# Kernel optimization log

Hardware: AMD Instinct MI355X
Metric: run time of the kernel (lower is better)

## Reference

```python
import jax, jax.numpy as jnp
import numpy as np

NUM_EMBED = 1024
NUM_HEADS = 16
NUM_LAYER = 8
BLOCK_SIZE = 1024
VOCAB = 32000
B, T = 4, 1024
HEAD_SIZE = NUM_EMBED // NUM_HEADS


def _ln(x, g, b, eps=1e-5):
    mu = jnp.mean(x, axis=-1, keepdims=True)
    var = jnp.var(x, axis=-1, keepdims=True)
    return (x - mu) * jax.lax.rsqrt(var + eps) * g + b


def setup_inputs() -> dict:
    key = jax.random.key(0)
    ks = jax.random.split(key, 16)
    C, L, V = NUM_EMBED, NUM_LAYER, VOCAB
    std = 0.02
    n = lambda k, shp: jax.random.normal(k, shp, jnp.float32) * std
    return {
        "x": jax.random.randint(ks[0], (B, T), 0, V),
        "tok_emb": n(ks[1], (V, C)),
        "pos_emb": n(ks[2], (BLOCK_SIZE, C)),
        "Wq": n(ks[3], (L, C, C)),
        "Wk": n(ks[4], (L, C, C)),
        "Wv": n(ks[5], (L, C, C)),
        "Wproj": n(ks[6], (L, C, C)),
        "bproj": jnp.zeros((L, C), jnp.float32),
        "ln1_g": jnp.ones((L, C), jnp.float32),
        "ln1_b": jnp.zeros((L, C), jnp.float32),
        "ln2_g": jnp.ones((L, C), jnp.float32),
        "ln2_b": jnp.zeros((L, C), jnp.float32),
        "W1": n(ks[7], (L, C, 4 * C)),
        "b1": jnp.zeros((L, 4 * C), jnp.float32),
        "W2": n(ks[8], (L, 4 * C, C)),
        "b2": jnp.zeros((L, C), jnp.float32),
        "lnf_g": jnp.ones((C,), jnp.float32),
        "lnf_b": jnp.zeros((C,), jnp.float32),
        "Whead": n(ks[9], (C, V)),
    }


def _forward(x, tok_emb, pos_emb, Wq, Wk, Wv, Wproj, bproj,
             ln1_g, ln1_b, ln2_g, ln2_b, W1, b1, W2, b2,
             lnf_g, lnf_b, Whead):
    Bc, Tc = x.shape
    H, hs = NUM_HEADS, HEAD_SIZE
    h = tok_emb[x] + pos_emb[:Tc]  # [B,T,C]
    causal = jnp.tril(jnp.ones((Tc, Tc), bool))
    neg_inf = jnp.finfo(h.dtype).min
    for l in range(NUM_LAYER):
        xn = _ln(h, ln1_g[l], ln1_b[l])
        q = (xn @ Wq[l]).reshape(Bc, Tc, H, hs)
        k = (xn @ Wk[l]).reshape(Bc, Tc, H, hs)
        v = (xn @ Wv[l]).reshape(Bc, Tc, H, hs)
        att = jnp.einsum('bqhd,bkhd->bhqk', q, k) * (hs ** -0.5)
        att = jnp.where(causal, att, neg_inf)
        att = jax.nn.softmax(att, axis=-1)  # dropout p=0 in eval
        o = jnp.einsum('bhqk,bkhd->bqhd', att, v).reshape(Bc, Tc, H * hs)
        h = h + o @ Wproj[l] + bproj[l]
        xn = _ln(h, ln2_g[l], ln2_b[l])
        h = h + jax.nn.relu(xn @ W1[l] + b1[l]) @ W2[l] + b2[l]
    h = _ln(h, lnf_g, lnf_b)
    return h @ Whead  # logits [B,T,V]


def reference(x, tok_emb, pos_emb, Wq, Wk, Wv, Wproj, bproj,
              ln1_g, ln1_b, ln2_g, ln2_b, W1, b1, W2, b2,
              lnf_g, lnf_b, Whead):
    return _forward(x, tok_emb, pos_emb, Wq, Wk, Wv, Wproj, bproj,
                    ln1_g, ln1_b, ln2_g, ln2_b, W1, b1, W2, b2,
                    lnf_g, lnf_b, Whead)
```

## Files before the change

kernel.cpp:

```cpp
#include <hip/hip_runtime.h>
#include <stdint.h>
#include <stddef.h>

#define C_DIM 1024
#define T_DIM 1024
#define B_DIM 4
#define L_DIM 8
#define V_DIM 32000
#define HS 64
#define NHEAD 16
#define NROWS (B_DIM * T_DIM)
#define LDQ   3072
#define PROWS 65536

typedef __bf16 bf16_t;
typedef __attribute__((ext_vector_type(8))) __bf16 bf16x8;
typedef __attribute__((ext_vector_type(4))) __bf16 bf16x4;
typedef __attribute__((ext_vector_type(4))) float f32x4;
typedef unsigned int u32;
typedef unsigned short u16;

static __device__ __forceinline__ f32x4 mfma16(bf16x8 a, bf16x8 b, f32x4 c) {
    return __builtin_amdgcn_mfma_f32_16x16x32_bf16(a, b, c, 0, 0, 0);
}

static __device__ __forceinline__ void gl_lds16(const bf16_t* g, bf16_t* l) {
    __builtin_amdgcn_global_load_lds(
        (const __attribute__((address_space(1))) u32*)(const void*)g,
        (__attribute__((address_space(3))) u32*)(void*)l, 16, 0, 0);
}

__global__ __launch_bounds__(256) void embed_kernel(
    const int* __restrict__ x, const float* __restrict__ tok,
    const float* __restrict__ pos, float* __restrict__ h) {
    int idx = blockIdx.x * 256 + threadIdx.x;
    int row = idx >> 8;
    int c4  = (idx & 255) * 4;
    int t   = row & (T_DIM - 1);
    int tk  = x[row];
    float4 a = *(const float4*)(tok + (size_t)tk * C_DIM + c4);
    float4 p = *(const float4*)(pos + (size_t)t * C_DIM + c4);
    float4 r;
    r.x = a.x + p.x; r.y = a.y + p.y; r.z = a.z + p.z; r.w = a.w + p.w;
    *(float4*)(h + (size_t)row * C_DIM + c4) = r;
}

static __device__ __forceinline__ void wtr_tile(
    const float* __restrict__ in, bf16_t* __restrict__ out,
    int K, int N, int n0, int k0, int tid) {
    __shared__ float t[64][65];
    int tx = tid & 63, tw = tid >> 6;
#pragma unroll 4
    for (int i = 0; i < 16; ++i) {
        int k = tw * 16 + i;
        t[k][tx] = in[(size_t)(k0 + k) * N + n0 + tx];
    }
    __syncthreads();
#pragma unroll 4
    for (int i = 0; i < 16; ++i) {
        int n = tw * 16 + i;
        out[(size_t)(n0 + n) * K + k0 + tx] = (bf16_t)t[tx][n];
    }
}

__global__ __launch_bounds__(256) void wtr_kernel(
    const float* __restrict__ in, bf16_t* __restrict__ out, int K, int N) {
    wtr_tile(in, out, K, N, blockIdx.x * 64, blockIdx.y * 64, threadIdx.x);
}

__global__ __launch_bounds__(256) void wtr_layer_kernel(
    const float* __restrict__ Wq, const float* __restrict__ Wk,
    const float* __restrict__ Wv, const float* __restrict__ Wp,
    const float* __restrict__ W1, const float* __restrict__ W2,
    bf16_t* __restrict__ qkvT, bf16_t* __restrict__ projT,
    bf16_t* __restrict__ w1T, bf16_t* __restrict__ w2T) {
    int b = blockIdx.x;
    const float* in; bf16_t* out; int K, N, tn, tk;
    if (b < 1024) {
        int which = b >> 8, t = b & 255;
        in  = which == 0 ? Wq : which == 1 ? Wk : which == 2 ? Wv : Wp;
        out = which < 3 ? qkvT + (size_t)which * C_DIM * C_DIM : projT;
        K = C_DIM; N = C_DIM; tn = t & 15; tk = t >> 4;
    } else if (b < 2048) {
        int t = b - 1024; in = W1; out = w1T;
        K = C_DIM; N = 4 * C_DIM; tn = t & 63; tk = t >> 6;
    } else {
        int t = b - 2048; in = W2; out = w2T;
        K = 4 * C_DIM; N = C_DIM; tn = t & 15; tk = t >> 4;
    }
    wtr_tile(in, out, K, N, tn * 64, tk * 64, threadIdx.x);
}

__global__ __launch_bounds__(256) void ln_kernel(
    const float* __restrict__ x, const float* __restrict__ gam,
    const float* __restrict__ bet, bf16_t* __restrict__ out) {
    int wave = threadIdx.x >> 6, lane = threadIdx.x & 63;
    int row  = blockIdx.x * 4 + wave;
    const float* xr = x + (size_t)row * C_DIM;
    float4 v[4];
    float s = 0.f, sq = 0.f;
#pragma unroll
    for (int i = 0; i < 4; ++i) {
        v[i] = *(const float4*)(xr + i * 256 + lane * 4);
        s  += v[i].x + v[i].y + v[i].z + v[i].w;
        sq += v[i].x * v[i].x + v[i].y * v[i].y + v[i].z * v[i].z + v[i].w * v[i].w;
    }
#pragma unroll
    for (int m = 1; m < 64; m <<= 1) {
        s  += __shfl_xor(s, m);
        sq += __shfl_xor(sq, m);
    }
    float mu  = s * (1.f / 1024.f);
    float var = sq * (1.f / 1024.f) - mu * mu;
    float rs  = rsqrtf(var + 1e-5f);
    bf16_t* orow = out + (size_t)row * C_DIM;
#pragma unroll
    for (int i = 0; i < 4; ++i) {
        int c = i * 256 + lane * 4;
        float4 g4 = *(const float4*)(gam + c);
        float4 b4 = *(const float4*)(bet + c);
        bf16x4 o;
        o[0] = (bf16_t)((v[i].x - mu) * rs * g4.x + b4.x);
        o[1] = (bf16_t)((v[i].y - mu) * rs * g4.y + b4.y);
        o[2] = (bf16_t)((v[i].z - mu) * rs * g4.z + b4.z);
        o[3] = (bf16_t)((v[i].w - mu) * rs * g4.w + b4.w);
        *(bf16x4*)(orow + c) = o;
    }
}

template <int MODE>
__global__ __launch_bounds__(256) void gemm_kernel(
    const bf16_t* __restrict__ A, const bf16_t* __restrict__ Bt,
    const float* __restrict__ bias, void* __restrict__ Cout,
    int M, int N, int K) {
    __shared__ bf16_t Asm[2][128 * 32];
    __shared__ bf16_t Bsm[2][128 * 32];

    const int tid  = threadIdx.x;
    const int nwg  = gridDim.x;
    int bid = blockIdx.x;
    if ((nwg & 7) == 0) {
        int cpx = nwg >> 3;
        bid = (bid & 7) * cpx + (bid >> 3);
    }
    const int MT = M >> 7;
    const int mt = bid % MT, nt = bid / MT;
    const int mbase = mt << 7, nbase = nt << 7;
    const int wave = tid >> 6, lane = tid & 63;
    const int lr = lane & 15, lg = lane >> 4;
    const int wm = wave >> 1, wn = wave & 1;
    const int NK = K >> 5;

    const int srow = lane >> 2;
    const int ssw  = (((lane & 3) ^ ((lane >> 3) & 3)) << 3);
    const bf16_t* aRow = A  + (size_t)(mbase + wave * 32 + srow) * K + ssw;
    const bf16_t* bRow = Bt + (size_t)(nbase + wave * 32 + srow) * K + ssw;
    const int ldsW = wave * 1024;

#define STAGE(buf, kt)                                                        \
    do {                                                                      \
        const bf16_t* ag = aRow + (size_t)(kt) * 32;                          \
        const bf16_t* bg = bRow + (size_t)(kt) * 32;                          \
        gl_lds16(ag,            &Asm[buf][ldsW]);                             \
        gl_lds16(ag + 16 * K,   &Asm[buf][ldsW + 512]);                       \
        gl_lds16(bg,            &Bsm[buf][ldsW]);                             \
        gl_lds16(bg + 16 * K,   &Bsm[buf][ldsW + 512]);                       \
    } while (0)

    STAGE(0, 0);
    __syncthreads();

    f32x4 acc[4][4] = {};
    const int rsw = ((lg ^ ((lr >> 1) & 3)) << 3);
    int buf = 0;
    for (int kt = 0; kt < NK; ++kt) {
        if (kt + 1 < NK) STAGE(buf ^ 1, kt + 1);
        bf16x8 af[4], bfr[4];
#pragma unroll
        for (int i = 0; i < 4; ++i)
            af[i] = *(const bf16x8*)&Asm[buf][(wm * 64 + i * 16 + lr) * 32 + rsw];
#pragma unroll
        for (int j = 0; j < 4; ++j)
            bfr[j] = *(const bf16x8*)&Bsm[buf][(wn * 64 + j * 16 + lr) * 32 + rsw];
#pragma unroll
        for (int i = 0; i < 4; ++i)
#pragma unroll
            for (int j = 0; j < 4; ++j)
                acc[i][j] = mfma16(af[i], bfr[j], acc[i][j]);
        __syncthreads();
        buf ^= 1;
    }
#undef STAGE

    float bj[4];
#pragma unroll
    for (int j = 0; j < 4; ++j)
        bj[j] = bias ? bias[nbase + wn * 64 + j * 16 + lr] : 0.0f;
#pragma unroll
    for (int i = 0; i < 4; ++i) {
#pragma unroll
        for (int j = 0; j < 4; ++j) {
            int col = nbase + wn * 64 + j * 16 + lr;
#pragma unroll
            for (int e = 0; e < 4; ++e) {
                int row = mbase + wm * 64 + i * 16 + lg * 4 + e;
                float val = acc[i][j][e] + bj[j];
                size_t off = (size_t)row * N + col;
                if (MODE == 0) {
                    ((bf16_t*)Cout)[off] = (bf16_t)val;
                } else if (MODE == 1) {
                    ((bf16_t*)Cout)[off] = (bf16_t)fmaxf(val, 0.0f);
                } else if (MODE == 2) {
                    ((float*)Cout)[off] += val;
                } else {
                    __builtin_nontemporal_store(val, &((float*)Cout)[off]);
                }
            }
        }
    }
}

template <int MODE>
__global__ __launch_bounds__(512, 4) void gemmW_kernel(
    const bf16_t* __restrict__ A, const bf16_t* __restrict__ Bt,
    const float* __restrict__ bias, void* __restrict__ Cout,
    int M, int N, int K) {
    __shared__ bf16_t As[2][128 * 32];
    __shared__ bf16_t Bs[2][256 * 32];

    const int tid  = threadIdx.x;
    const int nwg  = gridDim.x;
    int bid = blockIdx.x;
    if ((nwg & 7) == 0) {
        int cpx = nwg >> 3;
        bid = (bid & 7) * cpx + (bid >> 3);
    }
    const int MT = M >> 7;
    const int mt = bid % MT, nt = bid / MT;
    const int mbase = mt << 7, nbase = nt << 8;
    const int wave = tid >> 6, lane = tid & 63;
    const int lr = lane & 15, lg = lane >> 4;
    const int wm64 = (wave >> 2) * 64;
    const int wn64 = (wave & 3) * 64;
    const int NK = K >> 5;

    const int srow = tid >> 2;
    const int csrc = (((tid & 3) ^ ((tid >> 3) & 3)) << 3);
    const bf16_t* aPtr = A  + (size_t)(mbase + srow) * K + csrc;
    const bf16_t* b0   = Bt + (size_t)(nbase + srow) * K + csrc;
    const bf16_t* b1   = b0 + (size_t)128 * K;
    const int ldsW = wave * 512;

#define STAGEW(buf, kt)                                                       \
    do {                                                                      \
        gl_lds16(aPtr + (size_t)(kt) * 32, &As[buf][ldsW]);                   \
        gl_lds16(b0   + (size_t)(kt) * 32, &Bs[buf][ldsW]);                   \
        gl_lds16(b1   + (size_t)(kt) * 32, &Bs[buf][4096 + ldsW]);            \
    } while (0)

    STAGEW(0, 0);
    __syncthreads();

    f32x4 acc[4][4] = {};
    const int rofs = ((lg ^ ((lr >> 1) & 3)) << 3);
    int buf = 0;
    for (int kt = 0; kt < NK; ++kt) {
        if (kt + 1 < NK) STAGEW(buf ^ 1, kt + 1);
        bf16x8 af[4], bfr[4];
#pragma unroll
        for (int i = 0; i < 4; ++i)
            af[i] = *(const bf16x8*)&As[buf][(wm64 + i * 16 + lr) * 32 + rofs];
#pragma unroll
        for (int j = 0; j < 4; ++j)
            bfr[j] = *(const bf16x8*)&Bs[buf][(wn64 + j * 16 + lr) * 32 + rofs];
#pragma unroll
        for (int i = 0; i < 4; ++i)
#pragma unroll
            for (int j = 0; j < 4; ++j)
                acc[i][j] = mfma16(af[i], bfr[j], acc[i][j]);
        __syncthreads();
        buf ^= 1;
    }
#undef STAGEW

    float bj[4];
#pragma unroll
    for (int j = 0; j < 4; ++j)
        bj[j] = bias ? bias[nbase + wn64 + j * 16 + lr] : 0.0f;
#pragma unroll
    for (int i = 0; i < 4; ++i) {
#pragma unroll
        for (int j = 0; j < 4; ++j) {
            int col = nbase + wn64 + j * 16 + lr;
#pragma unroll
            for (int e = 0; e < 4; ++e) {
                int row = mbase + wm64 + i * 16 + lg * 4 + e;
                float val = acc[i][j][e] + bj[j];
                size_t off = (size_t)row * N + col;
                if (MODE == 0) {
                    ((bf16_t*)Cout)[off] = (bf16_t)val;
                } else if (MODE == 1) {
                    ((bf16_t*)Cout)[off] = (bf16_t)fmaxf(val, 0.0f);
                } else {
                    __builtin_nontemporal_store(val, &((float*)Cout)[off]);
                }
            }
        }
    }
}

__global__ __launch_bounds__(256) void attn_kernel(
    const bf16_t* __restrict__ Qb, const bf16_t* __restrict__ Kb,
    const bf16_t* __restrict__ Vb, float* __restrict__ Opart,
    float* __restrict__ Lbuf) {
    __shared__ bf16_t Ksm[2][64][72];
    __shared__ bf16_t Vsm[2][64][72];
    __shared__ bf16_t Psm[4][32][72];

    const int tid  = threadIdx.x;
    const int bid  = blockIdx.x;
    const int rank = bid >> 6;
    const int qt   = 7 - (rank >> 1);
    const int half = rank & 1;
    const int bh   = bid & 63;
    const int hh   = bh & 15;
    const int bb   = bh >> 4;
    const int t0   = half ? (qt + 1) : 0;
    const int t1   = half ? (2 * qt + 2) : (qt + 1);
    const int wave = tid >> 6, lane = tid & 63;
    const int lr = lane & 15, lg = lane >> 4;
    const int qbase = qt * 128 + wave * 32;
    const size_t basei = ((size_t)bb * T_DIM) * LDQ + hh * HS;
    const int pg = bh * 8 + qt;

    bf16x8 qf[2][2];
#pragma unroll
    for (int rb = 0; rb < 2; ++rb) {
        const bf16_t* qrow = Qb + basei + (size_t)(qbase + rb * 16 + lr) * LDQ;
        qf[rb][0] = *(const bf16x8*)(qrow + lg * 8);
        qf[rb][1] = *(const bf16x8*)(qrow + 32 + lg * 8);
    }

    f32x4 o[2][4] = {};
    float psum[2][4];
#pragma unroll
    for (int rb = 0; rb < 2; ++rb)
#pragma unroll
        for (int e = 0; e < 4; ++e) psum[rb][e] = 0.f;

    const int krow = tid >> 2, kc = (tid & 3) * 8;
    const bf16_t* kgp = Kb + basei + (size_t)krow * LDQ + kc;
    const int vds = (tid & 7) * 8, vkg = (tid >> 3) * 2;
    const bf16_t* vgp0 = Vb + basei + (size_t)vkg * LDQ + vds;
    const bf16_t* vgp1 = vgp0 + LDQ;

    uint4 k0r, k1r, v0r, v1r;
    {
        const size_t g0 = (size_t)t0 * 64 * LDQ;
        k0r = *(const uint4*)(kgp + g0);
        k1r = *(const uint4*)(kgp + g0 + 32);
        v0r = *(const uint4*)(vgp0 + g0);
        v1r = *(const uint4*)(vgp1 + g0);
    }
    *(uint4*)&Ksm[0][krow][kc]      = k0r;
    *(uint4*)&Ksm[0][krow][kc + 32] = k1r;
    {
        const u16* e0 = (const u16*)&v0r;
        const u16* e1 = (const u16*)&v1r;
#pragma unroll
        for (int j = 0; j < 8; ++j)
            *(u32*)&Vsm[0][vds + j][vkg] = (u32)e0[j] | ((u32)e1[j] << 16);
    }
    __syncthreads();

    const float SCL = 0.18033688011112042f;
    for (int kt = t0; kt < t1; ++kt) {
        const int c = (kt - t0) & 1;
        if (kt + 1 < t1) {
            const size_t go = (size_t)(kt + 1) * 64 * LDQ;
            k0r = *(const uint4*)(kgp + go);
            k1r = *(const uint4*)(kgp + go + 32);
            v0r = *(const uint4*)(vgp0 + go);
            v1r = *(const uint4*)(vgp1 + go);
        }

        f32x4 s[2][4];
        __builtin_amdgcn_s_setprio(1);
#pragma unroll
        for (int kk = 0; kk < 4; ++kk) {
            bf16x8 kf0 = *(const bf16x8*)&Ksm[c][kk * 16 + lr][lg * 8];
            bf16x8 kf1 = *(const bf16x8*)&Ksm[c][kk * 16 + lr][32 + lg * 8];
#pragma unroll
            for (int rb = 0; rb < 2; ++rb) {
                f32x4 z = {};
                z = mfma16(qf[rb][0], kf0, z);
                z = mfma16(qf[rb][1], kf1, z);
                s[rb][kk] = z;
            }
        }
        __builtin_amdgcn_s_setprio(0);
        if (kt * 64 + 63 > qbase) {
#pragma unroll
            for (int rb = 0; rb < 2; ++rb)
#pragma unroll
                for (int kk = 0; kk < 4; ++kk)
#pragma unroll
                    for (int e = 0; e < 4; ++e) {
                        int key = kt * 64 + kk * 16 + lr;
                        int qi  = qbase + rb * 16 + lg * 4 + e;
                        float v = s[rb][kk][e] * SCL;
                        s[rb][kk][e] = (key <= qi) ? v : -1e30f;
                    }
        } else {
#pragma unroll
            for (int rb = 0; rb < 2; ++rb)
#pragma unroll
                for (int kk = 0; kk < 4; ++kk)
#pragma unroll
                    for (int e = 0; e < 4; ++e)
                        s[rb][kk][e] *= SCL;
        }

#pragma unroll
        for (int rb = 0; rb < 2; ++rb) {
#pragma unroll
            for (int e = 0; e < 4; ++e) {
                float p0 = exp2f(s[rb][0][e]);
                float p1 = exp2f(s[rb][1][e]);
                float p2 = exp2f(s[rb][2][e]);
                float p3 = exp2f(s[rb][3][e]);
                int qrow = rb * 16 + lg * 4 + e;
                Psm[wave][qrow][lr]      = (bf16_t)p0;
                Psm[wave][qrow][16 + lr] = (bf16_t)p1;
                Psm[wave][qrow][32 + lr] = (bf16_t)p2;
                Psm[wave][qrow][48 + lr] = (bf16_t)p3;
                psum[rb][e] += (p0 + p1) + (p2 + p3);
            }
        }

        asm volatile("s_waitcnt lgkmcnt(0)" ::: "memory");
        bf16x8 pf[2][2];
#pragma unroll
        for (int rb = 0; rb < 2; ++rb)
#pragma unroll
            for (int h2 = 0; h2 < 2; ++h2)
                pf[rb][h2] = *(const bf16x8*)&Psm[wave][rb * 16 + lr][h2 * 32 + lg * 8];
        __builtin_amdgcn_s_setprio(1);
#pragma unroll
        for (int h2 = 0; h2 < 2; ++h2)
#pragma unroll
            for (int db = 0; db < 4; ++db) {
                bf16x8 vf = *(const bf16x8*)&Vsm[c][db * 16 + lr][h2 * 32 + lg * 8];
#pragma unroll
                for (int rb = 0; rb < 2; ++rb)
                    o[rb][db] = mfma16(pf[rb][h2], vf, o[rb][db]);
            }
        __builtin_amdgcn_s_setprio(0);

        if (kt + 1 < t1) {
            const int w = c ^ 1;
            *(uint4*)&Ksm[w][krow][kc]      = k0r;
            *(uint4*)&Ksm[w][krow][kc + 32] = k1r;
            const u16* e0 = (const u16*)&v0r;
            const u16* e1 = (const u16*)&v1r;
#pragma unroll
            for (int j = 0; j < 8; ++j)
                *(u32*)&Vsm[w][vds + j][vkg] = (u32)e0[j] | ((u32)e1[j] << 16);
        }
        __syncthreads();
    }

    const size_t prow0 = (size_t)half * PROWS + (size_t)pg * 128 + wave * 32;
#pragma unroll
    for (int rb = 0; rb < 2; ++rb)
#pragma unroll
        for (int e = 0; e < 4; ++e) {
            float l = psum[rb][e];
            l += __shfl_xor(l, 1);
            l += __shfl_xor(l, 2);
            l += __shfl_xor(l, 4);
            l += __shfl_xor(l, 8);
            size_t row = prow0 + rb * 16 + lg * 4 + e;
            float* op = Opart + row * 64;
#pragma unroll
            for (int db = 0; db < 4; ++db)
                op[db * 16 + lr] = o[rb][db][e];
            if (lr == 0) Lbuf[row] = l;
        }
}

__global__ __launch_bounds__(256) void attn_merge_kernel(
    const float* __restrict__ Opart, const float* __restrict__ Lbuf,
    bf16_t* __restrict__ Ob) {
    int idx = blockIdx.x * 256 + threadIdx.x;
    int row = idx >> 6, d = idx & 63;
    float l0 = Lbuf[row];
    float l1 = Lbuf[(size_t)PROWS + row];
    float inv = 1.0f / (l0 + l1);
    float v = (Opart[(size_t)row * 64 + d] +
               Opart[((size_t)PROWS + row) * 64 + d]) * inv;
    int pg = row >> 7, rloc = row & 127;
    int bh = pg >> 3, qt = pg & 7;
    int bb = bh >> 4, hh = bh & 15;
    Ob[((size_t)bb * T_DIM + qt * 128 + rloc) * C_DIM + hh * HS + d] = (bf16_t)v;
}

extern "C" void kernel_launch(void* const* d_in, const int* in_sizes, int n_in,
                              void* d_out, int out_size, void* d_ws, size_t ws_size,
                              hipStream_t stream) {
    const int*   x      = (const int*)d_in[0];
    const float* tok    = (const float*)d_in[1];
    const float* pos    = (const float*)d_in[2];
    const float* Wq     = (const float*)d_in[3];
    const float* Wk     = (const float*)d_in[4];
    const float* Wv     = (const float*)d_in[5];
    const float* Wproj  = (const float*)d_in[6];
    const float* bproj  = (const float*)d_in[7];
    const float* ln1_g  = (const float*)d_in[8];
    const float* ln1_b  = (const float*)d_in[9];
    const float* ln2_g  = (const float*)d_in[10];
    const float* ln2_b  = (const float*)d_in[11];
    const float* W1     = (const float*)d_in[12];
    const float* b1     = (const float*)d_in[13];
    const float* W2     = (const float*)d_in[14];
    const float* b2     = (const float*)d_in[15];
    const float* lnf_g  = (const float*)d_in[16];
    const float* lnf_b  = (const float*)d_in[17];
    const float* Whead  = (const float*)d_in[18];
    float* out = (float*)d_out;

    char* ws = (char*)d_ws;
    float*  h    = (float*)ws;   ws += (size_t)NROWS * C_DIM * 4;
    bf16_t* xn   = (bf16_t*)ws;  ws += (size_t)NROWS * C_DIM * 2;
    bf16_t* qkvb = (bf16_t*)ws;  ws += (size_t)NROWS * LDQ * 2;
    bf16_t* ob   = (bf16_t*)ws;  ws += (size_t)NROWS * C_DIM * 2;
    bf16_t* mid  = (bf16_t*)ws;  ws += (size_t)NROWS * 4 * C_DIM * 2;
    bf16_t* wT   = (bf16_t*)ws;  ws += (size_t)V_DIM * C_DIM * 2;
    float*  opart = (float*)ws;  ws += (size_t)2 * PROWS * 64 * 4;
    float*  lbuf  = (float*)ws;  ws += (size_t)2 * PROWS * 4;

    const size_t M1 = (size_t)C_DIM * C_DIM;
    bf16_t* qkvT  = wT;
    bf16_t* projT = wT + 3 * M1;
    bf16_t* w1T   = wT + 4 * M1;
    bf16_t* w2T   = wT + 8 * M1;

    dim3 blk(256);
    dim3 blk512(512);

    embed_kernel<<<dim3(NROWS * C_DIM / 1024), blk, 0, stream>>>(x, tok, pos, h);

    for (int l = 0; l < L_DIM; ++l) {
        const size_t wo  = (size_t)l * M1;
        const size_t wo1 = (size_t)l * 4 * M1;

        wtr_layer_kernel<<<dim3(3072), blk, 0, stream>>>(
            Wq + wo, Wk + wo, Wv + wo, Wproj + wo, W1 + wo1, W2 + wo1,
            qkvT, projT, w1T, w2T);

        ln_kernel<<<dim3(NROWS / 4), blk, 0, stream>>>(h, ln1_g + l * C_DIM, ln1_b + l * C_DIM, xn);

        gemmW_kernel<0><<<dim3(32 * 12), blk512, 0, stream>>>(
            xn, qkvT, nullptr, qkvb, NROWS, LDQ, C_DIM);

        attn_kernel<<<dim3(1024), blk, 0, stream>>>(
            qkvb, qkvb + C_DIM, qkvb + 2 * C_DIM, opart, lbuf);
        attn_merge_kernel<<<dim3(PROWS * 64 / 256), blk, 0, stream>>>(
            opart, lbuf, ob);

        gemm_kernel<2><<<dim3(32 * 8), blk, 0, stream>>>(ob, projT, bproj + l * C_DIM, h, NROWS, C_DIM, C_DIM);

        ln_kernel<<<dim3(NROWS / 4), blk, 0, stream>>>(h, ln2_g + l * C_DIM, ln2_b + l * C_DIM, xn);

        gemmW_kernel<1><<<dim3(32 * 16), blk512, 0, stream>>>(
            xn, w1T, b1 + (size_t)l * 4 * C_DIM, mid, NROWS, 4 * C_DIM, C_DIM);
        gemm_kernel<2><<<dim3(32 * 8), blk, 0, stream>>>(mid, w2T, b2 + l * C_DIM, h, NROWS, C_DIM, 4 * C_DIM);
    }

    ln_kernel<<<dim3(NROWS / 4), blk, 0, stream>>>(h, lnf_g, lnf_b, xn);
    wtr_kernel<<<dim3(500, 16), blk, 0, stream>>>(Whead, wT, C_DIM, V_DIM);
    gemmW_kernel<3><<<dim3(32 * 125), blk512, 0, stream>>>(
        xn, wT, nullptr, out, NROWS, V_DIM, C_DIM);
}
```

Baseline: 2.530 ms.

## Overlap weight transposes with attention via extra blocks and double-buffered weights

Weight transpose/convert work is moved off the critical path. Layer 0 weights are transposed in a kernel fused with the embedding. Each later layer's weights are transposed by extra blocks appended to the previous layer's attention kernel, and the head weights by extra blocks in the last attention launch. Two weight buffers alternate between layers so the next layer's weights can be written while the current ones are in use. The attention merge is also vectorised to float4 loads and bf16x4 stores. The cost is more workspace, a larger shared-memory union in the attention kernel that may lower occupancy, and the transpose blocks competing with attention for compute units.

```diff
diff --git a/kernel.cpp b/kernel.cpp
--- a/kernel.cpp
+++ b/kernel.cpp
@@ -30,25 +30,9 @@
         (__attribute__((address_space(3))) u32*)(void*)l, 16, 0, 0);
 }
 
-__global__ __launch_bounds__(256) void embed_kernel(
-    const int* __restrict__ x, const float* __restrict__ tok,
-    const float* __restrict__ pos, float* __restrict__ h) {
-    int idx = blockIdx.x * 256 + threadIdx.x;
-    int row = idx >> 8;
-    int c4  = (idx & 255) * 4;
-    int t   = row & (T_DIM - 1);
-    int tk  = x[row];
-    float4 a = *(const float4*)(tok + (size_t)tk * C_DIM + c4);
-    float4 p = *(const float4*)(pos + (size_t)t * C_DIM + c4);
-    float4 r;
-    r.x = a.x + p.x; r.y = a.y + p.y; r.z = a.z + p.z; r.w = a.w + p.w;
-    *(float4*)(h + (size_t)row * C_DIM + c4) = r;
-}
-
-static __device__ __forceinline__ void wtr_tile(
-    const float* __restrict__ in, bf16_t* __restrict__ out,
+static __device__ __forceinline__ void wtr_tile_p(
+    float (*t)[65], const float* __restrict__ in, bf16_t* __restrict__ out,
     int K, int N, int n0, int k0, int tid) {
-    __shared__ float t[64][65];
     int tx = tid & 63, tw = tid >> 6;
 #pragma unroll 4
     for (int i = 0; i < 16; ++i) {
@@ -63,32 +47,52 @@
     }
 }
 
-__global__ __launch_bounds__(256) void wtr_kernel(
-    const float* __restrict__ in, bf16_t* __restrict__ out, int K, int N) {
-    wtr_tile(in, out, K, N, blockIdx.x * 64, blockIdx.y * 64, threadIdx.x);
-}
-
-__global__ __launch_bounds__(256) void wtr_layer_kernel(
+static __device__ __forceinline__ void wtr_layer_block(
+    float (*t)[65], int b,
+    const float* Wq, const float* Wk, const float* Wv, const float* Wp,
+    const float* W1, const float* W2,
+    bf16_t* qkvT, bf16_t* projT, bf16_t* w1T, bf16_t* w2T, int tid) {
+    const float* in; bf16_t* out; int K, N, tn, tk;
+    if (b < 1024) {
+        int which = b >> 8, tt = b & 255;
+        in  = which == 0 ? Wq : which == 1 ? Wk : which == 2 ? Wv : Wp;
+        out = which < 3 ? qkvT + (size_t)which * C_DIM * C_DIM : projT;
+        K = C_DIM; N = C_DIM; tn = tt & 15; tk = tt >> 4;
+    } else if (b < 2048) {
+        int tt = b - 1024; in = W1; out = w1T;
+        K = C_DIM; N = 4 * C_DIM; tn = tt & 63; tk = tt >> 6;
+    } else {
+        int tt = b - 2048; in = W2; out = w2T;
+        K = 4 * C_DIM; N = C_DIM; tn = tt & 15; tk = tt >> 4;
+    }
+    wtr_tile_p(t, in, out, K, N, tn * 64, tk * 64, tid);
+}
+
+__global__ __launch_bounds__(256) void embed_wtr_kernel(
+    const int* __restrict__ x, const float* __restrict__ tok,
+    const float* __restrict__ pos, float* __restrict__ h,
     const float* __restrict__ Wq, const float* __restrict__ Wk,
     const float* __restrict__ Wv, const float* __restrict__ Wp,
     const float* __restrict__ W1, const float* __restrict__ W2,
     bf16_t* __restrict__ qkvT, bf16_t* __restrict__ projT,
     bf16_t* __restrict__ w1T, bf16_t* __restrict__ w2T) {
-    int b = blockIdx.x;
-    const float* in; bf16_t* out; int K, N, tn, tk;
-    if (b < 1024) {
-        int which = b >> 8, t = b & 255;
-        in  = which == 0 ? Wq : which == 1 ? Wk : which == 2 ? Wv : Wp;
-        out = which < 3 ? qkvT + (size_t)which * C_DIM * C_DIM : projT;
-        K = C_DIM; N = C_DIM; tn = t & 15; tk = t >> 4;
-    } else if (b < 2048) {
-        int t = b - 1024; in = W1; out = w1T;
-        K = C_DIM; N = 4 * C_DIM; tn = t & 63; tk = t >> 6;
+    __shared__ float t[64][65];
+    int bid = blockIdx.x;
+    if (bid < 4096) {
+        int idx = bid * 256 + threadIdx.x;
+        int row = idx >> 8;
+        int c4  = (idx & 255) * 4;
+        int tt  = row & (T_DIM - 1);
+        int tk  = x[row];
+        float4 a = *(const float4*)(tok + (size_t)tk * C_DIM + c4);
+        float4 p = *(const float4*)(pos + (size_t)tt * C_DIM + c4);
+        float4 r;
+        r.x = a.x + p.x; r.y = a.y + p.y; r.z = a.z + p.z; r.w = a.w + p.w;
+        *(float4*)(h + (size_t)row * C_DIM + c4) = r;
     } else {
-        int t = b - 2048; in = W2; out = w2T;
-        K = 4 * C_DIM; N = C_DIM; tn = t & 15; tk = t >> 4;
-    }
-    wtr_tile(in, out, K, N, tn * 64, tk * 64, threadIdx.x);
+        wtr_layer_block(t, bid - 4096, Wq, Wk, Wv, Wp, W1, W2,
+                        qkvT, projT, w1T, w2T, threadIdx.x);
+    }
 }
 
 __global__ __launch_bounds__(256) void ln_kernel(
@@ -312,13 +316,33 @@
 __global__ __launch_bounds__(256) void attn_kernel(
     const bf16_t* __restrict__ Qb, const bf16_t* __restrict__ Kb,
     const bf16_t* __restrict__ Vb, float* __restrict__ Opart,
-    float* __restrict__ Lbuf) {
-    __shared__ bf16_t Ksm[2][64][72];
-    __shared__ bf16_t Vsm[2][64][72];
-    __shared__ bf16_t Psm[4][32][72];
-
-    const int tid  = threadIdx.x;
-    const int bid  = blockIdx.x;
+    float* __restrict__ Lbuf, int aux,
+    const float* __restrict__ xWq, const float* __restrict__ xWk,
+    const float* __restrict__ xWv, const float* __restrict__ xWp,
+    const float* __restrict__ xW1, const float* __restrict__ xW2,
+    bf16_t* __restrict__ oQkv, bf16_t* __restrict__ oProj,
+    bf16_t* __restrict__ oW1, bf16_t* __restrict__ oW2) {
+    __shared__ __align__(16) char smem[55296];
+    const int tid = threadIdx.x;
+    const int bid = blockIdx.x;
+
+    if (bid >= 1024) {
+        float (*t)[65] = (float(*)[65])smem;
+        int b = bid - 1024;
+        if (aux == 1) {
+            wtr_layer_block(t, b, xWq, xWk, xWv, xWp, xW1, xW2,
+                            oQkv, oProj, oW1, oW2, tid);
+        } else {
+            int tn = b % 500, tk = b / 500;
+            wtr_tile_p(t, xWq, oQkv, C_DIM, V_DIM, tn * 64, tk * 64, tid);
+        }
+        return;
+    }
+
+    bf16_t (*Ksm)[64][72] = (bf16_t(*)[64][72])smem;
+    bf16_t (*Vsm)[64][72] = (bf16_t(*)[64][72])(smem + 18432);
+    bf16_t (*Psm)[32][72] = (bf16_t(*)[32][72])(smem + 36864);
+
     const int rank = bid >> 6;
     const int qt   = 7 - (rank >> 1);
     const int half = rank & 1;
@@ -493,16 +517,21 @@
     const float* __restrict__ Opart, const float* __restrict__ Lbuf,
     bf16_t* __restrict__ Ob) {
     int idx = blockIdx.x * 256 + threadIdx.x;
-    int row = idx >> 6, d = idx & 63;
+    int row = idx >> 4, d4 = (idx & 15) * 4;
     float l0 = Lbuf[row];
     float l1 = Lbuf[(size_t)PROWS + row];
     float inv = 1.0f / (l0 + l1);
-    float v = (Opart[(size_t)row * 64 + d] +
-               Opart[((size_t)PROWS + row) * 64 + d]) * inv;
+    float4 a = *(const float4*)&Opart[(size_t)row * 64 + d4];
+    float4 b = *(const float4*)&Opart[((size_t)PROWS + row) * 64 + d4];
+    bf16x4 r;
+    r[0] = (bf16_t)((a.x + b.x) * inv);
+    r[1] = (bf16_t)((a.y + b.y) * inv);
+    r[2] = (bf16_t)((a.z + b.z) * inv);
+    r[3] = (bf16_t)((a.w + b.w) * inv);
     int pg = row >> 7, rloc = row & 127;
     int bh = pg >> 3, qt = pg & 7;
     int bb = bh >> 4, hh = bh & 15;
-    Ob[((size_t)bb * T_DIM + qt * 128 + rloc) * C_DIM + hh * HS + d] = (bf16_t)v;
+    *(bf16x4*)&Ob[((size_t)bb * T_DIM + qt * 128 + rloc) * C_DIM + hh * HS + d4] = r;
 }
 
 extern "C" void kernel_launch(void* const* d_in, const int* in_sizes, int n_in,
@@ -529,43 +558,53 @@
     const float* Whead  = (const float*)d_in[18];
     float* out = (float*)d_out;
 
+    const size_t M1 = (size_t)C_DIM * C_DIM;
     char* ws = (char*)d_ws;
     float*  h    = (float*)ws;   ws += (size_t)NROWS * C_DIM * 4;
     bf16_t* xn   = (bf16_t*)ws;  ws += (size_t)NROWS * C_DIM * 2;
     bf16_t* qkvb = (bf16_t*)ws;  ws += (size_t)NROWS * LDQ * 2;
     bf16_t* ob   = (bf16_t*)ws;  ws += (size_t)NROWS * C_DIM * 2;
     bf16_t* mid  = (bf16_t*)ws;  ws += (size_t)NROWS * 4 * C_DIM * 2;
-    bf16_t* wT   = (bf16_t*)ws;  ws += (size_t)V_DIM * C_DIM * 2;
+    bf16_t* wb0  = (bf16_t*)ws;  ws += 12 * M1 * 2;
+    bf16_t* wb1  = (bf16_t*)ws;  ws += 12 * M1 * 2;
+    bf16_t* headT = (bf16_t*)ws; ws += (size_t)V_DIM * C_DIM * 2;
     float*  opart = (float*)ws;  ws += (size_t)2 * PROWS * 64 * 4;
     float*  lbuf  = (float*)ws;  ws += (size_t)2 * PROWS * 4;
 
-    const size_t M1 = (size_t)C_DIM * C_DIM;
-    bf16_t* qkvT  = wT;
-    bf16_t* projT = wT + 3 * M1;
-    bf16_t* w1T   = wT + 4 * M1;
-    bf16_t* w2T   = wT + 8 * M1;
-
     dim3 blk(256);
     dim3 blk512(512);
 
-    embed_kernel<<<dim3(NROWS * C_DIM / 1024), blk, 0, stream>>>(x, tok, pos, h);
+    embed_wtr_kernel<<<dim3(4096 + 3072), blk, 0, stream>>>(
+        x, tok, pos, h, Wq, Wk, Wv, Wproj, W1, W2,
+        wb0, wb0 + 3 * M1, wb0 + 4 * M1, wb0 + 8 * M1);
 
     for (int l = 0; l < L_DIM; ++l) {
-        const size_t wo  = (size_t)l * M1;
-        const size_t wo1 = (size_t)l * 4 * M1;
-
-        wtr_layer_kernel<<<dim3(3072), blk, 0, stream>>>(
-            Wq + wo, Wk + wo, Wv + wo, Wproj + wo, W1 + wo1, W2 + wo1,
-            qkvT, projT, w1T, w2T);
+        bf16_t* lw = (l & 1) ? wb1 : wb0;
+        bf16_t* nw = (l & 1) ? wb0 : wb1;
+        bf16_t* qkvT  = lw;
+        bf16_t* projT = lw + 3 * M1;
+        bf16_t* w1T   = lw + 4 * M1;
+        bf16_t* w2T   = lw + 8 * M1;
 
         ln_kernel<<<dim3(NROWS / 4), blk, 0, stream>>>(h, ln1_g + l * C_DIM, ln1_b + l * C_DIM, xn);
 
         gemmW_kernel<0><<<dim3(32 * 12), blk512, 0, stream>>>(
             xn, qkvT, nullptr, qkvb, NROWS, LDQ, C_DIM);
 
-        attn_kernel<<<dim3(1024), blk, 0, stream>>>(
-            qkvb, qkvb + C_DIM, qkvb + 2 * C_DIM, opart, lbuf);
-        attn_merge_kernel<<<dim3(PROWS * 64 / 256), blk, 0, stream>>>(
+        if (l < 7) {
+            const size_t wo  = (size_t)(l + 1) * M1;
+            const size_t wo1 = (size_t)(l + 1) * 4 * M1;
+            attn_kernel<<<dim3(1024 + 3072), blk, 0, stream>>>(
+                qkvb, qkvb + C_DIM, qkvb + 2 * C_DIM, opart, lbuf, 1,
+                Wq + wo, Wk + wo, Wv + wo, Wproj + wo, W1 + wo1, W2 + wo1,
+                nw, nw + 3 * M1, nw + 4 * M1, nw + 8 * M1);
+        } else {
+            attn_kernel<<<dim3(1024 + 8000), blk, 0, stream>>>(
+                qkvb, qkvb + C_DIM, qkvb + 2 * C_DIM, opart, lbuf, 2,
+                Whead, nullptr, nullptr, nullptr, nullptr, nullptr,
+                headT, nullptr, nullptr, nullptr);
+        }
+        attn_merge_kernel<<<dim3(PROWS * 16 / 256), blk, 0, stream>>>(
             opart, lbuf, ob);
 
         gemm_kernel<2><<<dim3(32 * 8), blk, 0, stream>>>(ob, projT, bproj + l * C_DIM, h, NROWS, C_DIM, C_DIM);
@@ -578,7 +617,6 @@
     }
 
     ln_kernel<<<dim3(NROWS / 4), blk, 0, stream>>>(h, lnf_g, lnf_b, xn);
-    wtr_kernel<<<dim3(500, 16), blk, 0, stream>>>(Whead, wT, C_DIM, V_DIM);
     gemmW_kernel<3><<<dim3(32 * 125), blk512, 0, stream>>>(
-        xn, wT, nullptr, out, NROWS, V_DIM, C_DIM);
-}
+        xn, headT, nullptr, out, NROWS, V_DIM, C_DIM);
+}
```

Result: no change. 2.573 ms (+1.7%).
